# Performance work log

Hardware: AMD Instinct MI355X
Metric: run time of the kernel (lower is better)

The kernel has to match this reference:

```python
import jax, jax.numpy as jnp
import numpy as np


def setup_inputs() -> dict:
    key = jax.random.key(0)
    ks = jax.random.split(key, 10)
    B, HD, CD = 8192, 1024, 1024
    stdv = 1.0 / np.sqrt(HD)
    inp = {
        "hprev": jax.random.normal(ks[0], (B, HD), dtype=jnp.float32),
        "cprev": jax.random.normal(ks[1], (B, CD), dtype=jnp.float32),
        "w_hi": jax.random.uniform(ks[2], (HD, CD), jnp.float32, -stdv, stdv),
        "b_hi": jax.random.uniform(ks[3], (1, CD), jnp.float32, -stdv, stdv),
        "w_hf": jax.random.uniform(ks[4], (HD, CD), jnp.float32, -stdv, stdv),
        "b_hf": jax.random.uniform(ks[5], (1, CD), jnp.float32, -stdv, stdv),
        "w_hg": jax.random.uniform(ks[6], (HD, CD), jnp.float32, -stdv, stdv),
        "b_hg": jax.random.uniform(ks[7], (1, CD), jnp.float32, -stdv, stdv),
        "w_ho": jax.random.uniform(ks[8], (HD, CD), jnp.float32, -stdv, stdv),
        "b_ho": jax.random.uniform(ks[9], (1, CD), jnp.float32, -stdv, stdv),
    }
    return inp


def reference(hprev, cprev, w_hi, b_hi, w_hf, b_hf, w_hg, b_hg, w_ho, b_ho):
    # LSTM cell gates driven only by previous hidden state.
    i = jax.nn.sigmoid(hprev @ w_hi + b_hi)   # input gate  [B, CD]
    f = jax.nn.sigmoid(hprev @ w_hf + b_hf)   # forget gate [B, CD]
    g = jnp.tanh(hprev @ w_hg + b_hg)         # cell candidate
    o = jax.nn.sigmoid(hprev @ w_ho + b_ho)   # output gate
    cprime = f * cprev + i * g
    hprime = o * jnp.tanh(cprime)
    return (hprime, cprime)
```

## Files before the change

kernel.cpp:

```cpp
#include <hip/hip_runtime.h>
#include <hip/hip_bf16.h>
#include <stdint.h>

typedef short short8 __attribute__((ext_vector_type(8)));
typedef float f32x4 __attribute__((ext_vector_type(4)));
typedef unsigned short ushort4v __attribute__((ext_vector_type(4)));

#define MDIM 8192
#define KDIM 1024
#define NDIM 1024
#define NHALF 32


__device__ __forceinline__ unsigned short f2bf(float f) {
  union { float f; unsigned int u; } v; v.f = f;
  unsigned int u = v.u;
  u += 0x7fffu + ((u >> 16) & 1u);
  return (unsigned short)(u >> 16);
}

__device__ __forceinline__ void load_lds16(const void* gsrc, void* ldst) {
  __builtin_amdgcn_global_load_lds(
      (__attribute__((address_space(1))) void*)gsrc,
      (__attribute__((address_space(3))) void*)ldst,
      16, 0, 0);
}

__device__ __forceinline__ float fast_sigmoid(float x) {
  return 1.0f / (1.0f + __expf(-x));
}

__device__ __forceinline__ float fast_tanh(float x) {
  x = fminf(30.0f, fmaxf(-30.0f, x));
  float e = __expf(-2.0f * x);
  return (1.0f - e) / (1.0f + e);
}


__global__ void convert_h_kernel(const float* __restrict__ in,
                                 unsigned short* __restrict__ out, int n4) {
  int idx = blockIdx.x * blockDim.x + threadIdx.x;
  int stride = gridDim.x * blockDim.x;
  for (int i = idx; i < n4; i += stride) {
    float4 v = reinterpret_cast<const float4*>(in)[i];
    ushort4v o;
    o.x = f2bf(v.x); o.y = f2bf(v.y); o.z = f2bf(v.z); o.w = f2bf(v.w);
    reinterpret_cast<ushort4v*>(out)[i] = o;
  }
}

__global__ void convert_w_kernel(const float* __restrict__ w0,
                                 const float* __restrict__ w1,
                                 const float* __restrict__ w2,
                                 const float* __restrict__ w3,
                                 unsigned short* __restrict__ wT) {
  __shared__ float tile[64][65];
  int g = blockIdx.z;
  const float* w = (g == 0) ? w0 : (g == 1) ? w1 : (g == 2) ? w2 : w3;
  int k0 = blockIdx.y * 64;
  int n0 = blockIdx.x * 64;
  int tx = threadIdx.x;
  int ty = threadIdx.y;
#pragma unroll
  for (int j = 0; j < 16; ++j) {
    int kk = ty * 16 + j;
    tile[kk][tx] = w[(size_t)(k0 + kk) * NDIM + n0 + tx];
  }
  __syncthreads();
  unsigned short* dst = wT + (size_t)g * NDIM * KDIM;
#pragma unroll
  for (int j = 0; j < 16; ++j) {
    int nn = ty * 16 + j;
    dst[(size_t)(n0 + nn) * KDIM + k0 + tx] = f2bf(tile[tx][nn]);
  }
}


#define SLOT_SZ 32768
#define S0 0
#define S1 32768
#define S2 65536
#define S3 98304

#define BARRIER() __builtin_amdgcn_s_barrier()
#define WAIT_LGKM0() do { \
    asm volatile("s_waitcnt lgkmcnt(0)" ::: "memory"); \
    __builtin_amdgcn_sched_barrier(0); } while (0)
#define WAIT_VM8() asm volatile("s_waitcnt vmcnt(8)" ::: "memory")

#define STAGE_A_H(koff, T) do { \
    load_lds16(hb + srcA0 + (koff), lds + (T) + tid * 16); \
    load_lds16(hb + srcA1 + (koff), lds + (T) + 8192 + tid * 16); } while (0)
#define STAGE_B_H(koff, T) do { \
    load_lds16(wb + srcB0 + (koff), lds + (T) + 16384 + tid * 16); \
    load_lds16(wb + srcB1 + (koff), lds + (T) + 16384 + 8192 + tid * 16); } while (0)

#define MFMA16(mb_) do { \
  _Pragma("unroll") \
  for (int mi = 0; mi < 4; ++mi) { \
    _Pragma("unroll") \
    for (int g = 0; g < 4; ++g) \
      acc[g][(mb_) + mi] = __builtin_amdgcn_mfma_f32_16x16x32_bf16( \
          Af[mi], Bf[g], acc[g][(mb_) + mi], 0, 0, 0); \
  } } while (0)

#define HALF(hidx, S, T) do { \
    const uint32_t ko = (uint32_t)(((hidx) + 3) & (NHALF - 1)) * 64; \
     \
    short8 Bf[4], Af[4]; \
    _Pragma("unroll") \
    for (int g = 0; g < 4; ++g) \
      Bf[g] = *(const short8*)(lds + (S) + 16384 + g * 4096 + b_off); \
    _Pragma("unroll") \
    for (int mi = 0; mi < 4; ++mi) \
      Af[mi] = *(const short8*)(lds + (S) + a_off + mi * 1024); \
    STAGE_A_H(ko, T); \
    BARRIER(); \
    WAIT_LGKM0(); \
    __builtin_amdgcn_s_setprio(1); \
    MFMA16(0); \
    __builtin_amdgcn_s_setprio(0); \
    BARRIER(); \
     \
    _Pragma("unroll") \
    for (int mi = 0; mi < 4; ++mi) \
      Af[mi] = *(const short8*)(lds + (S) + a_off + (4 + mi) * 1024); \
    STAGE_B_H(ko, T); \
    BARRIER(); \
    WAIT_LGKM0(); \
    __builtin_amdgcn_s_setprio(1); \
    MFMA16(4); \
    __builtin_amdgcn_s_setprio(0); \
    WAIT_VM8(); \
    BARRIER(); } while (0)

__global__ __launch_bounds__(512, 2) void lstm_fused_gemm(
    const unsigned short* __restrict__ hbf,
    const unsigned short* __restrict__ wT,
    const float* __restrict__ cprev,
    const float* __restrict__ b_i, const float* __restrict__ b_f,
    const float* __restrict__ b_g, const float* __restrict__ b_o,
    float* __restrict__ out)
{
  extern __shared__ unsigned char lds[];
  const int tid  = threadIdx.x;
  const int lane = tid & 63;
  const int wave = tid >> 6;
  const int wr = wave >> 2;
  const int wc = wave & 3;
  const int r15 = lane & 15;
  const int hh  = lane >> 4;

  int bid = blockIdx.x;
  int loc = bid >> 3;
  int mb = (bid & 7) * 4 + (loc >> 4);
  int nb = loc & 15;
  int brow = mb * 256;
  int bcol = nb * 64;

  const char* hb = (const char*)hbf;
  const char* wb = (const char*)wT;

  const int sD = tid & 7;
  const int pB = tid >> 3;
  const int u  = sD ^ (pB & 7);
  const int c16 = (u & 3) * 16;
  const int rA0 = 2 * pB + (u >> 2);
  const int rA1 = 128 + rA0;
  const uint32_t srcA0 = (uint32_t)(brow + rA0) * 2048 + c16;
  const uint32_t srcA1 = (uint32_t)(brow + rA1) * 2048 + c16;
  const uint32_t srcB0 = (uint32_t)((rA0 >> 6) * 1024 + bcol + (rA0 & 63)) * 2048 + c16;
  const uint32_t srcB1 = (uint32_t)((rA1 >> 6) * 1024 + bcol + (rA1 & 63)) * 2048 + c16;

  const int slot16 = (((((r15 & 1) << 2) | hh) ^ (r15 >> 1)) * 16);
  const uint32_t a_off = (uint32_t)(wr * 64 + (r15 >> 1)) * 128 + slot16;
  const uint32_t b_off = (uint32_t)(wc * 8 + (r15 >> 1)) * 128 + slot16;

  f32x4 acc[4][8];
#pragma unroll
  for (int g = 0; g < 4; ++g)
#pragma unroll
    for (int m = 0; m < 8; ++m)
      acc[g][m] = (f32x4){0.f, 0.f, 0.f, 0.f};

  STAGE_A_H(0, S0);       STAGE_B_H(0, S0);
  STAGE_A_H(64, S1);      STAGE_B_H(64, S1);
  STAGE_A_H(128, S2);     STAGE_B_H(128, S2);
  WAIT_VM8();
  BARRIER();

  for (int h = 0; h < NHALF; h += 4) {
    HALF(h + 0, S0, S3);
    HALF(h + 1, S1, S0);
    HALF(h + 2, S2, S1);
    HALF(h + 3, S3, S2);
  }

  const size_t outC = (size_t)MDIM * NDIM;
  const int cc = bcol + wc * 16 + r15;
  const float bi = b_i[cc], bff = b_f[cc], bg = b_g[cc], bo = b_o[cc];
#pragma unroll
  for (int m = 0; m < 8; ++m) {
#pragma unroll
    for (int j = 0; j < 4; ++j) {
      int rr = brow + wr * 128 + m * 16 + hh * 4 + j;
      size_t base = (size_t)rr * NDIM + cc;
      float pi = acc[0][m][j] + bi;
      float pf = acc[1][m][j] + bff;
      float pg = acc[2][m][j] + bg;
      float po = acc[3][m][j] + bo;
      float iv = fast_sigmoid(pi);
      float fv = fast_sigmoid(pf);
      float gv = fast_tanh(pg);
      float ov = fast_sigmoid(po);
      float cp = fv * cprev[base] + iv * gv;
      float hp = ov * fast_tanh(cp);
      out[base] = hp;
      out[outC + base] = cp;
    }
  }
}


extern "C" void kernel_launch(void* const* d_in, const int* in_sizes, int n_in,
                              void* d_out, int out_size, void* d_ws, size_t ws_size,
                              hipStream_t stream) {
  const float* hprev = (const float*)d_in[0];
  const float* cprev = (const float*)d_in[1];
  const float* w_hi  = (const float*)d_in[2];
  const float* b_hi  = (const float*)d_in[3];
  const float* w_hf  = (const float*)d_in[4];
  const float* b_hf  = (const float*)d_in[5];
  const float* w_hg  = (const float*)d_in[6];
  const float* b_hg  = (const float*)d_in[7];
  const float* w_ho  = (const float*)d_in[8];
  const float* b_ho  = (const float*)d_in[9];
  float* out = (float*)d_out;

  unsigned short* hbf = (unsigned short*)d_ws;
  unsigned short* wT  = (unsigned short*)((char*)d_ws + (size_t)MDIM * KDIM * 2);

  convert_h_kernel<<<2048, 256, 0, stream>>>(hprev, hbf, MDIM * KDIM / 4);
  convert_w_kernel<<<dim3(16, 16, 4), dim3(64, 4, 1), 0, stream>>>(
      w_hi, w_hf, w_hg, w_ho, wT);
  lstm_fused_gemm<<<512, 512, 131072, stream>>>(hbf, wT, cprev,
                                                b_hi, b_hf, b_hg, b_ho, out);
}
```

Measured before the change: 101.2 us.

## Pre-tile bf16 operands into K-panel layout and use double-buffered 64-wide K tiles

The conversion kernels now write hprev and the transposed weights into K-tiled panels of 64 columns, so each K step reads one contiguous 128-byte row per matrix row. The GEMM moves from a 4-slot pipeline over 32-wide K halves to a 2-buffer pipeline over 64-wide K tiles, with a new XOR swizzle and a full vmcnt(0) wait per tile. The goal is more contiguous global-to-LDS loads and fewer barriers per K step. The cost is a shallower prefetch depth, which may expose more load latency.

```diff
diff --git a/kernel.cpp b/kernel.cpp
--- a/kernel.cpp
+++ b/kernel.cpp
@@ -9,7 +9,7 @@
 #define MDIM 8192
 #define KDIM 1024
 #define NDIM 1024
-#define NHALF 32
+#define NKT  16
 
 
 __device__ __forceinline__ unsigned short f2bf(float f) {
@@ -37,27 +37,36 @@
 }
 
 
-__global__ void convert_h_kernel(const float* __restrict__ in,
-                                 unsigned short* __restrict__ out, int n4) {
+__global__ void convert_h_tiled(const float* __restrict__ in,
+                                unsigned short* __restrict__ out, int nchunk) {
   int idx = blockIdx.x * blockDim.x + threadIdx.x;
   int stride = gridDim.x * blockDim.x;
-  for (int i = idx; i < n4; i += stride) {
-    float4 v = reinterpret_cast<const float4*>(in)[i];
-    ushort4v o;
-    o.x = f2bf(v.x); o.y = f2bf(v.y); o.z = f2bf(v.z); o.w = f2bf(v.w);
-    reinterpret_cast<ushort4v*>(out)[i] = o;
-  }
-}
-
-__global__ void convert_w_kernel(const float* __restrict__ w0,
-                                 const float* __restrict__ w1,
-                                 const float* __restrict__ w2,
-                                 const float* __restrict__ w3,
-                                 unsigned short* __restrict__ wT) {
+  for (int i = idx; i < nchunk; i += stride) {
+    int r = i >> 7;
+    int kc8 = i & 127;
+    const float4* src = reinterpret_cast<const float4*>(in + (size_t)r * KDIM + kc8 * 8);
+    float4 v0 = src[0], v1 = src[1];
+    short8 o;
+    o[0] = (short)f2bf(v0.x); o[1] = (short)f2bf(v0.y);
+    o[2] = (short)f2bf(v0.z); o[3] = (short)f2bf(v0.w);
+    o[4] = (short)f2bf(v1.x); o[5] = (short)f2bf(v1.y);
+    o[6] = (short)f2bf(v1.z); o[7] = (short)f2bf(v1.w);
+    int kt = kc8 >> 3;
+    int c8 = kc8 & 7;
+    reinterpret_cast<short8*>(out)[((size_t)kt * MDIM + r) * 8 + c8] = o;
+  }
+}
+
+__global__ void convert_w_tiled(const float* __restrict__ w0,
+                                const float* __restrict__ w1,
+                                const float* __restrict__ w2,
+                                const float* __restrict__ w3,
+                                unsigned short* __restrict__ out) {
   __shared__ float tile[64][65];
   int g = blockIdx.z;
   const float* w = (g == 0) ? w0 : (g == 1) ? w1 : (g == 2) ? w2 : w3;
-  int k0 = blockIdx.y * 64;
+  int kt = blockIdx.y;
+  int k0 = kt * 64;
   int n0 = blockIdx.x * 64;
   int tx = threadIdx.x;
   int ty = threadIdx.y;
@@ -67,33 +76,32 @@
     tile[kk][tx] = w[(size_t)(k0 + kk) * NDIM + n0 + tx];
   }
   __syncthreads();
-  unsigned short* dst = wT + (size_t)g * NDIM * KDIM;
 #pragma unroll
   for (int j = 0; j < 16; ++j) {
     int nn = ty * 16 + j;
-    dst[(size_t)(n0 + nn) * KDIM + k0 + tx] = f2bf(tile[tx][nn]);
-  }
-}
-
-
-#define SLOT_SZ 32768
-#define S0 0
-#define S1 32768
-#define S2 65536
-#define S3 98304
+    out[(((size_t)kt * 4 + g) * NDIM + n0 + nn) * 64 + tx] = f2bf(tile[tx][nn]);
+  }
+}
+
+
+#define BUF0 0
+#define BUF1 65536
 
 #define BARRIER() __builtin_amdgcn_s_barrier()
 #define WAIT_LGKM0() do { \
     asm volatile("s_waitcnt lgkmcnt(0)" ::: "memory"); \
     __builtin_amdgcn_sched_barrier(0); } while (0)
-#define WAIT_VM8() asm volatile("s_waitcnt vmcnt(8)" ::: "memory")
-
-#define STAGE_A_H(koff, T) do { \
-    load_lds16(hb + srcA0 + (koff), lds + (T) + tid * 16); \
-    load_lds16(hb + srcA1 + (koff), lds + (T) + 8192 + tid * 16); } while (0)
-#define STAGE_B_H(koff, T) do { \
-    load_lds16(wb + srcB0 + (koff), lds + (T) + 16384 + tid * 16); \
-    load_lds16(wb + srcB1 + (koff), lds + (T) + 16384 + 8192 + tid * 16); } while (0)
+#define WAIT_VM0() asm volatile("s_waitcnt vmcnt(0)" ::: "memory")
+
+#define STAGE_A2(T, kA, j0) do { \
+    load_lds16(ab + srcA + (kA) + (j0) * 8192,       lds + (T) + (j0) * 8192 + tid * 16); \
+    load_lds16(ab + srcA + (kA) + ((j0) + 1) * 8192, lds + (T) + ((j0) + 1) * 8192 + tid * 16); } while (0)
+#define STAGE_B2(T, kB, j0) do { \
+    load_lds16(bb + srcB + (kB) + (j0) * 131072,       lds + (T) + 32768 + (j0) * 8192 + tid * 16); \
+    load_lds16(bb + srcB + (kB) + ((j0) + 1) * 131072, lds + (T) + 32768 + ((j0) + 1) * 8192 + tid * 16); } while (0)
+
+#define RD_A(S, m, s) (*(const short8*)(lds + (S) + a_base + (m) * 2048 + (s)))
+#define RD_B(S, g, s) (*(const short8*)(lds + (S) + b_base + (g) * 8192 + (s)))
 
 #define MFMA16(mb_) do { \
   _Pragma("unroll") \
@@ -104,39 +112,37 @@
           Af[mi], Bf[g], acc[g][(mb_) + mi], 0, 0, 0); \
   } } while (0)
 
-#define HALF(hidx, S, T) do { \
-    const uint32_t ko = (uint32_t)(((hidx) + 3) & (NHALF - 1)) * 64; \
-     \
-    short8 Bf[4], Af[4]; \
-    _Pragma("unroll") \
-    for (int g = 0; g < 4; ++g) \
-      Bf[g] = *(const short8*)(lds + (S) + 16384 + g * 4096 + b_off); \
-    _Pragma("unroll") \
-    for (int mi = 0; mi < 4; ++mi) \
-      Af[mi] = *(const short8*)(lds + (S) + a_off + mi * 1024); \
-    STAGE_A_H(ko, T); \
+#define TILE(CUR, NXT, kA, kB) do { \
+    short8 Af[4], Bf[4]; \
+     \
+    _Pragma("unroll") for (int g = 0; g < 4; ++g) Bf[g] = RD_B(CUR, g, s0); \
+    _Pragma("unroll") for (int mi = 0; mi < 4; ++mi) Af[mi] = RD_A(CUR, mi, s0); \
+    STAGE_A2(NXT, kA, 0); STAGE_A2(NXT, kA, 2); \
+    BARRIER(); WAIT_LGKM0(); \
+    __builtin_amdgcn_s_setprio(1); MFMA16(0); __builtin_amdgcn_s_setprio(0); \
     BARRIER(); \
-    WAIT_LGKM0(); \
-    __builtin_amdgcn_s_setprio(1); \
-    MFMA16(0); \
-    __builtin_amdgcn_s_setprio(0); \
+     \
+    _Pragma("unroll") for (int mi = 0; mi < 4; ++mi) Af[mi] = RD_A(CUR, 4 + mi, s0); \
+    STAGE_B2(NXT, kB, 0); STAGE_B2(NXT, kB, 2); \
+    BARRIER(); WAIT_LGKM0(); \
+    __builtin_amdgcn_s_setprio(1); MFMA16(4); __builtin_amdgcn_s_setprio(0); \
     BARRIER(); \
      \
-    _Pragma("unroll") \
-    for (int mi = 0; mi < 4; ++mi) \
-      Af[mi] = *(const short8*)(lds + (S) + a_off + (4 + mi) * 1024); \
-    STAGE_B_H(ko, T); \
+    _Pragma("unroll") for (int g = 0; g < 4; ++g) Bf[g] = RD_B(CUR, g, s1); \
+    _Pragma("unroll") for (int mi = 0; mi < 4; ++mi) Af[mi] = RD_A(CUR, mi, s1); \
+    BARRIER(); WAIT_LGKM0(); \
+    __builtin_amdgcn_s_setprio(1); MFMA16(0); __builtin_amdgcn_s_setprio(0); \
     BARRIER(); \
-    WAIT_LGKM0(); \
-    __builtin_amdgcn_s_setprio(1); \
-    MFMA16(4); \
-    __builtin_amdgcn_s_setprio(0); \
-    WAIT_VM8(); \
+     \
+    _Pragma("unroll") for (int mi = 0; mi < 4; ++mi) Af[mi] = RD_A(CUR, 4 + mi, s1); \
+    BARRIER(); WAIT_LGKM0(); \
+    __builtin_amdgcn_s_setprio(1); MFMA16(4); __builtin_amdgcn_s_setprio(0); \
+    WAIT_VM0(); \
     BARRIER(); } while (0)
 
 __global__ __launch_bounds__(512, 2) void lstm_fused_gemm(
-    const unsigned short* __restrict__ hbf,
-    const unsigned short* __restrict__ wT,
+    const unsigned short* __restrict__ At,
+    const unsigned short* __restrict__ Bt,
     const float* __restrict__ cprev,
     const float* __restrict__ b_i, const float* __restrict__ b_f,
     const float* __restrict__ b_g, const float* __restrict__ b_o,
@@ -158,23 +164,18 @@
   int brow = mb * 256;
   int bcol = nb * 64;
 
-  const char* hb = (const char*)hbf;
-  const char* wb = (const char*)wT;
-
-  const int sD = tid & 7;
-  const int pB = tid >> 3;
-  const int u  = sD ^ (pB & 7);
-  const int c16 = (u & 3) * 16;
-  const int rA0 = 2 * pB + (u >> 2);
-  const int rA1 = 128 + rA0;
-  const uint32_t srcA0 = (uint32_t)(brow + rA0) * 2048 + c16;
-  const uint32_t srcA1 = (uint32_t)(brow + rA1) * 2048 + c16;
-  const uint32_t srcB0 = (uint32_t)((rA0 >> 6) * 1024 + bcol + (rA0 & 63)) * 2048 + c16;
-  const uint32_t srcB1 = (uint32_t)((rA1 >> 6) * 1024 + bcol + (rA1 & 63)) * 2048 + c16;
-
-  const int slot16 = (((((r15 & 1) << 2) | hh) ^ (r15 >> 1)) * 16);
-  const uint32_t a_off = (uint32_t)(wr * 64 + (r15 >> 1)) * 128 + slot16;
-  const uint32_t b_off = (uint32_t)(wc * 8 + (r15 >> 1)) * 128 + slot16;
+  const char* ab = (const char*)At;
+  const char* bb = (const char*)Bt;
+
+  const int rloc = tid >> 3;
+  const int cx = (((tid & 7) ^ (rloc & 7)) << 4);
+  const uint32_t srcA = (uint32_t)(brow + rloc) * 128 + cx;
+  const uint32_t srcB = (uint32_t)(bcol + rloc) * 128 + cx;
+
+  const int s0 = ((hh ^ (r15 & 7)) << 4);
+  const int s1 = s0 ^ 64;
+  const uint32_t a_base = (uint32_t)(wr * 128 + r15) * 128;
+  const uint32_t b_base = 32768u + (uint32_t)(wc * 16 + r15) * 128;
 
   f32x4 acc[4][8];
 #pragma unroll
@@ -183,17 +184,22 @@
     for (int m = 0; m < 8; ++m)
       acc[g][m] = (f32x4){0.f, 0.f, 0.f, 0.f};
 
-  STAGE_A_H(0, S0);       STAGE_B_H(0, S0);
-  STAGE_A_H(64, S1);      STAGE_B_H(64, S1);
-  STAGE_A_H(128, S2);     STAGE_B_H(128, S2);
-  WAIT_VM8();
+  STAGE_A2(BUF0, 0, 0); STAGE_A2(BUF0, 0, 2);
+  STAGE_B2(BUF0, 0, 0); STAGE_B2(BUF0, 0, 2);
+  WAIT_VM0();
   BARRIER();
 
-  for (int h = 0; h < NHALF; h += 4) {
-    HALF(h + 0, S0, S3);
-    HALF(h + 1, S1, S0);
-    HALF(h + 2, S2, S1);
-    HALF(h + 3, S3, S2);
+  for (int it = 0; it < NKT / 2; ++it) {
+    const uint32_t t1 = 2 * it + 1;
+    const uint32_t t2 = (2 * it + 2) & (NKT - 1);
+    {
+      const uint32_t kA = t1 << 20, kB = t1 << 19;
+      TILE(BUF0, BUF1, kA, kB);
+    }
+    {
+      const uint32_t kA = t2 << 20, kB = t2 << 19;
+      TILE(BUF1, BUF0, kA, kB);
+    }
   }
 
   const size_t outC = (size_t)MDIM * NDIM;
@@ -237,12 +243,12 @@
   const float* b_ho  = (const float*)d_in[9];
   float* out = (float*)d_out;
 
-  unsigned short* hbf = (unsigned short*)d_ws;
-  unsigned short* wT  = (unsigned short*)((char*)d_ws + (size_t)MDIM * KDIM * 2);
-
-  convert_h_kernel<<<2048, 256, 0, stream>>>(hprev, hbf, MDIM * KDIM / 4);
-  convert_w_kernel<<<dim3(16, 16, 4), dim3(64, 4, 1), 0, stream>>>(
-      w_hi, w_hf, w_hg, w_ho, wT);
-  lstm_fused_gemm<<<512, 512, 131072, stream>>>(hbf, wT, cprev,
+  unsigned short* At = (unsigned short*)d_ws;
+  unsigned short* Bt = (unsigned short*)((char*)d_ws + (size_t)NKT * MDIM * 64 * 2);
+
+  convert_h_tiled<<<2048, 256, 0, stream>>>(hprev, At, MDIM * KDIM / 8);
+  convert_w_tiled<<<dim3(16, 16, 4), dim3(64, 4, 1), 0, stream>>>(
+      w_hi, w_hf, w_hg, w_ho, Bt);
+  lstm_fused_gemm<<<512, 512, 131072, stream>>>(At, Bt, cprev,
                                                 b_hi, b_hf, b_hg, b_ho, out);
 }
```

Measured after the change: 99.60 us. Within noise of the previous version (-1.5%).
